# Kernel optimization log

Hardware: AMD Instinct MI355X
Metric: run time of the kernel (lower is better)

Reference implementation:

```python
import jax, jax.numpy as jnp
import numpy as np

# dims
B, T, C, D, H, NH, HD, INTER, L = 4, 1024, 256, 256, 512, 8, 64, 2048, 4
CF, CB, BASE = 0, 128, 10000.0  # context_forward, context_backward, rope theta


def _rope_tables():
    inv = 1.0 / (BASE ** (jnp.arange(0, HD, 2, dtype=jnp.float32) / HD))
    t = jnp.arange(T, dtype=jnp.float32)
    f = jnp.einsum('i,j->ij', t, inv)          # [T, HD/2]
    emb = jnp.concatenate([f, f], axis=-1)      # [T, HD]
    return jnp.cos(emb), jnp.sin(emb)


def _rotate_half(x):
    x1, x2 = jnp.split(x, 2, axis=-1)
    return jnp.concatenate([-x2, x1], axis=-1)


def _ln(x, g, b):
    m = x.mean(-1, keepdims=True)
    v = ((x - m) ** 2).mean(-1, keepdims=True)
    return (x - m) / jnp.sqrt(v + 1e-5) * g + b


def _band_mask():
    # create_context_mask(CF, CB, T): allow j in [i-CB, i+CF]
    i = jnp.arange(T)[:, None]
    j = jnp.arange(T)[None, :]
    return (j <= i + CF) & (j >= i - CB)  # [T, T] bool


def setup_inputs() -> dict:
    key = jax.random.key(0)
    ks = jax.random.split(key, 16)
    w = lambda k, shp: (0.02 * jax.random.normal(k, shp)).astype(jnp.float32)
    return {
        'spikes': jax.random.normal(ks[0], (B, T, C), dtype=jnp.float32),
        'spikes_mask': jnp.ones((B, T), dtype=jnp.int32),
        'spikes_timestamp': jnp.tile(jnp.arange(T, dtype=jnp.int32), (B, 1)),
        'embed_w': w(ks[1], (C, D)), 'embed_b': jnp.zeros((D,), jnp.float32),
        'proj_w': w(ks[2], (D, H)), 'proj_b': jnp.zeros((H,), jnp.float32),
        'ln1_g': jnp.ones((L, H), jnp.float32), 'ln1_b': jnp.zeros((L, H), jnp.float32),
        'Wq': w(ks[3], (L, H, H)), 'bq': jnp.zeros((L, H), jnp.float32),
        'Wk': w(ks[4], (L, H, H)), 'bk': jnp.zeros((L, H), jnp.float32),
        'Wv': w(ks[5], (L, H, H)), 'bv': jnp.zeros((L, H), jnp.float32),
        'Wo': w(ks[6], (L, H, H)), 'bo': jnp.zeros((L, H), jnp.float32),
        'ln2_g': jnp.ones((L, H), jnp.float32), 'ln2_b': jnp.zeros((L, H), jnp.float32),
        'up_w': w(ks[7], (L, H, INTER)), 'up_b': jnp.zeros((L, INTER), jnp.float32),
        'down_w': w(ks[8], (L, INTER, H)), 'down_b': jnp.zeros((L, H), jnp.float32),
    }


def reference(spikes, spikes_mask, spikes_timestamp, embed_w, embed_b, proj_w, proj_b,
              ln1_g, ln1_b, Wq, bq, Wk, bk, Wv, bv, Wo, bo, ln2_g, ln2_b,
              up_w, up_b, down_w, down_b):
    cos, sin = _rope_tables()
    mask = _band_mask()[None, None] & (spikes_mask[:, None, None, :] > 0)  # [B,1,T,T]
    cs = cos[spikes_timestamp][:, None]  # [B,1,T,HD]
    sn = sin[spikes_timestamp][:, None]
    neg = jnp.finfo(jnp.float32).min

    # NeuralEmbeddingLayer (no stack/pos/tokens): Linear -> gelu -> Linear
    x = jax.nn.gelu(spikes @ embed_w + embed_b, approximate=False) @ proj_w + proj_b

    for l in range(L):
        h = _ln(x, ln1_g[l], ln1_b[l])
        q = (h @ Wq[l] + bq[l]).reshape(B, T, NH, HD).transpose(0, 2, 1, 3)
        k = (h @ Wk[l] + bk[l]).reshape(B, T, NH, HD).transpose(0, 2, 1, 3)
        v = (h @ Wv[l] + bv[l]).reshape(B, T, NH, HD).transpose(0, 2, 1, 3)
        q = q * cs + _rotate_half(q) * sn
        k = k * cs + _rotate_half(k) * sn
        s = jnp.einsum('bhqd,bhkd->bhqk', q, k) / np.float32(np.sqrt(HD))
        s = jnp.where(mask, s, neg)
        p = jax.nn.softmax(s, axis=-1)
        o = jnp.einsum('bhqk,bhkd->bhqd', p, v).transpose(0, 2, 1, 3).reshape(B, T, H)
        x = x + o @ Wo[l] + bo[l]
        h = _ln(x, ln2_g[l], ln2_b[l])
        x = x + jax.nn.gelu(h @ up_w[l] + up_b[l], approximate=False) @ down_w[l] + down_b[l]
    return x
```

## Files before the change

### kernel.cpp

```cpp
#include <hip/hip_runtime.h>
#include <math.h>

#define B_ 4
#define T_ 1024
#define C_ 256
#define D_ 256
#define H_ 512
#define NH_ 8
#define HD_ 64
#define INTER_ 2048
#define L_ 4
#define CB_ 128

typedef short bf16x8 __attribute__((ext_vector_type(8)));
typedef float f32x4 __attribute__((ext_vector_type(4)));

__device__ __forceinline__ float gelu_exact(float x) {
    return 0.5f * x * (1.0f + erff(x * 0.70710678118654752f));
}

__device__ __forceinline__ unsigned short f2bf(float f) {
    unsigned u = __float_as_uint(f);
    u += 0x7fffu + ((u >> 16) & 1u);
    return (unsigned short)(u >> 16);
}
__device__ __forceinline__ float bf2f(unsigned short h) {
    return __uint_as_float((unsigned)h << 16);
}

__device__ __forceinline__ void xcd_swz(int& bx, int& by) {
    const int gx  = gridDim.x;
    const int nwg = gx * gridDim.y;
    int bid = blockIdx.y * gx + blockIdx.x;
    bid = (bid & 7) * (nwg >> 3) + (bid >> 3);
    bx = bid % gx;
    by = bid / gx;
}

template<int ACT, int RES, int OBF, int SPLIT>
__global__ __launch_bounds__(256) void mm64_k(
    const unsigned short* __restrict__ A, const unsigned short* __restrict__ BT,
    const float* __restrict__ b0, const float* __restrict__ b1,
    const float* __restrict__ b2,
    const float* res,
    void* o0, void* o1, void* o2,
    const int M, const int N, const int K)
{
    __shared__ unsigned short As[64 * 64];
    __shared__ unsigned short Bs[64 * 64];

    int bx, by; xcd_swz(bx, by);

    const int tid  = threadIdx.x;
    const int lane = tid & 63;
    const int w    = tid >> 6;
    const int m0   = by * 64;
    const int n0   = bx * 64;
    const int wm   = (w >> 1) * 32;
    const int wn   = (w & 1) * 32;
    const int l16  = lane & 15;
    const int g16  = lane >> 4;

    f32x4 acc[2][2] = {};

    const unsigned short* Abase = A  + (size_t)m0 * K;
    const unsigned short* Bbase = BT + (size_t)n0 * K;

    const int c0 = (w << 6) + lane;
    const int c1 = c0 + 256;
    const int r0c = c0 >> 3, g0c = c0 & 7, gk0 = g0c ^ (r0c & 7);
    const int r1c = c1 >> 3, g1c = c1 & 7, gk1 = g1c ^ (r1c & 7);

    for (int k0 = 0; k0 < K; k0 += 64) {
        __syncthreads();
        __builtin_amdgcn_global_load_lds(
            (const __attribute__((address_space(1))) unsigned*)(Abase + (size_t)r0c * K + k0 + gk0 * 8),
            (__attribute__((address_space(3))) unsigned*)(As + (size_t)(w << 6) * 8), 16, 0, 0);
        __builtin_amdgcn_global_load_lds(
            (const __attribute__((address_space(1))) unsigned*)(Abase + (size_t)r1c * K + k0 + gk1 * 8),
            (__attribute__((address_space(3))) unsigned*)(As + (size_t)(256 + (w << 6)) * 8), 16, 0, 0);
        __builtin_amdgcn_global_load_lds(
            (const __attribute__((address_space(1))) unsigned*)(Bbase + (size_t)r0c * K + k0 + gk0 * 8),
            (__attribute__((address_space(3))) unsigned*)(Bs + (size_t)(w << 6) * 8), 16, 0, 0);
        __builtin_amdgcn_global_load_lds(
            (const __attribute__((address_space(1))) unsigned*)(Bbase + (size_t)r1c * K + k0 + gk1 * 8),
            (__attribute__((address_space(3))) unsigned*)(Bs + (size_t)(256 + (w << 6)) * 8), 16, 0, 0);
        __syncthreads();

#pragma unroll
        for (int kk = 0; kk < 2; ++kk) {
            const int kf = kk * 4 + g16;
            const int sw = (kf ^ (l16 & 7)) * 8;
            bf16x8 a[2], b[2];
#pragma unroll
            for (int t = 0; t < 2; ++t)
                a[t] = *(const bf16x8*)&As[(wm + t * 16 + l16) * 64 + sw];
#pragma unroll
            for (int t = 0; t < 2; ++t)
                b[t] = *(const bf16x8*)&Bs[(wn + t * 16 + l16) * 64 + sw];
#pragma unroll
            for (int i = 0; i < 2; ++i)
#pragma unroll
                for (int j = 0; j < 2; ++j)
                    acc[i][j] = __builtin_amdgcn_mfma_f32_16x16x32_bf16(a[i], b[j], acc[i][j], 0, 0, 0);
        }
    }

    if (OBF || SPLIT) {
        __syncthreads();
        unsigned short* Eb = ((w < 2) ? As : Bs) + (w & 1) * 1024;
        const int row16 = lane >> 2;
        const int cg    = lane & 3;

        const int gnb   = n0 + wn;
        const int which = SPLIT ? (gnb >> 9) : 0;
        const int lnb   = SPLIT ? (gnb & 511) : gnb;
        const int ldo   = SPLIT ? 512 : N;
        unsigned short* oo = SPLIT
            ? ((which == 0) ? (unsigned short*)o0 : (which == 1) ? (unsigned short*)o1 : (unsigned short*)o2)
            : (unsigned short*)o0;
        const float* bb = SPLIT ? ((which == 0) ? b0 : (which == 1) ? b1 : b2) : b0;
        const float scale = (SPLIT && which == 0) ? 0.125f : 1.0f;

#pragma unroll
        for (int i = 0; i < 2; ++i) {
#pragma unroll
            for (int j = 0; j < 2; ++j) {
                const float bv = bb[lnb + j * 16 + l16];
#pragma unroll
                for (int r = 0; r < 4; ++r) {
                    float cv = acc[i][j][r] + bv;
                    if (ACT) cv = gelu_exact(cv);
                    if (SPLIT) cv *= scale;
                    Eb[(g16 * 4 + r) * 40 + j * 16 + l16] = f2bf(cv);
                }
            }
            const int grow0 = m0 + wm + i * 16 + row16;
#pragma unroll
            for (int s = 0; s < 2; ++s) {
                ushort4 t4 = *(const ushort4*)&Eb[row16 * 40 + s * 16 + cg * 4];
                *(ushort4*)&oo[(size_t)grow0 * ldo + lnb + s * 16 + cg * 4] = t4;
            }
        }
        return;
    }

#pragma unroll
    for (int i = 0; i < 2; ++i) {
        const int gmb = m0 + wm + i * 16 + g16 * 4;
#pragma unroll
        for (int j = 0; j < 2; ++j) {
            const int gn = n0 + wn + j * 16 + l16;
            const float bv = b0[gn];
#pragma unroll
            for (int r = 0; r < 4; ++r) {
                float cv = acc[i][j][r] + bv;
                if (ACT) cv = gelu_exact(cv);
                if (RES) cv += res[(size_t)(gmb + r) * 512 + gn];
                ((float*)o0)[(size_t)(gmb + r) * N + gn] = cv;
            }
        }
    }
}

template<int ACT, int RES, int OBF, int SPLIT>
__global__ __launch_bounds__(256) void mm128_k(
    const unsigned short* __restrict__ A, const unsigned short* __restrict__ BT,
    const float* __restrict__ b0, const float* __restrict__ b1,
    const float* __restrict__ b2,
    const float* res,
    void* o0, void* o1, void* o2,
    const int M, const int N, const int K)
{
    __shared__ unsigned short As[128 * 64];
    __shared__ unsigned short Bs[64 * 64];

    int bx, by; xcd_swz(bx, by);

    const int tid  = threadIdx.x;
    const int lane = tid & 63;
    const int w    = tid >> 6;
    const int m0   = by * 128;
    const int n0   = bx * 64;
    const int wm   = (w >> 1) * 64;
    const int wn   = (w & 1) * 32;
    const int l16  = lane & 15;
    const int g16  = lane >> 4;

    f32x4 acc[4][2] = {};

    const unsigned short* Abase = A  + (size_t)m0 * K;
    const unsigned short* Bbase = BT + (size_t)n0 * K;

    for (int k0 = 0; k0 < K; k0 += 64) {
        __syncthreads();
#pragma unroll
        for (int it = 0; it < 4; ++it) {
            const int c = it * 256 + tid;
            const int rc = c >> 3, gk = (c & 7) ^ (rc & 7);
            __builtin_amdgcn_global_load_lds(
                (const __attribute__((address_space(1))) unsigned*)(Abase + (size_t)rc * K + k0 + gk * 8),
                (__attribute__((address_space(3))) unsigned*)(As + (size_t)(it * 256 + (w << 6)) * 8), 16, 0, 0);
        }
#pragma unroll
        for (int it = 0; it < 2; ++it) {
            const int c = it * 256 + tid;
            const int rc = c >> 3, gk = (c & 7) ^ (rc & 7);
            __builtin_amdgcn_global_load_lds(
                (const __attribute__((address_space(1))) unsigned*)(Bbase + (size_t)rc * K + k0 + gk * 8),
                (__attribute__((address_space(3))) unsigned*)(Bs + (size_t)(it * 256 + (w << 6)) * 8), 16, 0, 0);
        }
        __syncthreads();

#pragma unroll
        for (int kk = 0; kk < 2; ++kk) {
            const int kf = kk * 4 + g16;
            const int sw = (kf ^ (l16 & 7)) * 8;
            bf16x8 a[4], b[2];
#pragma unroll
            for (int t = 0; t < 4; ++t)
                a[t] = *(const bf16x8*)&As[(wm + t * 16 + l16) * 64 + sw];
#pragma unroll
            for (int t = 0; t < 2; ++t)
                b[t] = *(const bf16x8*)&Bs[(wn + t * 16 + l16) * 64 + sw];
#pragma unroll
            for (int i = 0; i < 4; ++i)
#pragma unroll
                for (int j = 0; j < 2; ++j)
                    acc[i][j] = __builtin_amdgcn_mfma_f32_16x16x32_bf16(a[i], b[j], acc[i][j], 0, 0, 0);
        }
    }

    if (OBF || SPLIT) {
        __syncthreads();
        constexpr int EST = 40;
        unsigned short* Eb = As + w * (16 * EST);
        const int erow = lane >> 3;
        const int ecol = (lane & 7) * 4;

        const int gnb   = n0 + wn;
        const int which = SPLIT ? (gnb >> 9) : 0;
        const int lnb   = SPLIT ? (gnb & 511) : gnb;
        const int ldo   = SPLIT ? 512 : N;
        unsigned short* oo = SPLIT
            ? ((which == 0) ? (unsigned short*)o0 : (which == 1) ? (unsigned short*)o1 : (unsigned short*)o2)
            : (unsigned short*)o0;
        const float* bb = SPLIT ? ((which == 0) ? b0 : (which == 1) ? b1 : b2) : b0;
        const float scale = (SPLIT && which == 0) ? 0.125f : 1.0f;

#pragma unroll
        for (int i = 0; i < 4; ++i) {
#pragma unroll
            for (int j = 0; j < 2; ++j) {
                const float bv = bb[lnb + j * 16 + l16];
#pragma unroll
                for (int r = 0; r < 4; ++r) {
                    float cv = acc[i][j][r] + bv;
                    if (ACT) cv = gelu_exact(cv);
                    if (SPLIT) cv *= scale;
                    Eb[(g16 * 4 + r) * EST + j * 16 + l16] = f2bf(cv);
                }
            }
            const int grow0 = m0 + wm + i * 16;
#pragma unroll
            for (int s = 0; s < 2; ++s) {
                ushort4 t4 = *(const ushort4*)&Eb[(s * 8 + erow) * EST + ecol];
                *(ushort4*)&oo[(size_t)(grow0 + s * 8 + erow) * ldo + lnb + ecol] = t4;
            }
        }
        return;
    }

#pragma unroll
    for (int i = 0; i < 4; ++i) {
        const int gmb = m0 + wm + i * 16 + g16 * 4;
#pragma unroll
        for (int j = 0; j < 2; ++j) {
            const int gn = n0 + wn + j * 16 + l16;
            const float bv = b0[gn];
#pragma unroll
            for (int r = 0; r < 4; ++r) {
                float cv = acc[i][j][r] + bv;
                if (ACT) cv = gelu_exact(cv);
                if (RES) cv += res[(size_t)(gmb + r) * 512 + gn];
                ((float*)o0)[(size_t)(gmb + r) * N + gn] = cv;
            }
        }
    }
}

__global__ __launch_bounds__(256) void prep_k(
    const float* __restrict__ spikes,
    const float* __restrict__ embed_w, const float* __restrict__ proj_w,
    const float* __restrict__ Wq, const float* __restrict__ Wk,
    const float* __restrict__ Wv, const float* __restrict__ Wo,
    const float* __restrict__ up_w, const float* __restrict__ down_w,
    unsigned short* __restrict__ spbf,
    unsigned short* __restrict__ embT, unsigned short* __restrict__ projT,
    unsigned short* __restrict__ qkvT, unsigned short* __restrict__ woT,
    unsigned short* __restrict__ upT, unsigned short* __restrict__ downT)
{
    const int idx = blockIdx.x;
    const int tid = threadIdx.x;

    if (idx >= 3120) {
        const int base = (idx - 3120) * 4096 + tid * 16;
#pragma unroll
        for (int s = 0; s < 4; ++s) {
            float4 v = *(const float4*)&spikes[base + s * 4];
            ushort4 o = {f2bf(v.x), f2bf(v.y), f2bf(v.z), f2bf(v.w)};
            *(ushort4*)&spbf[base + s * 4] = o;
        }
        return;
    }

    const float* src; unsigned short* dst; int R, Cc, t;
    if (idx < 16)      { src = embed_w; dst = embT;  R = C_; Cc = D_; t = idx; }
    else if (idx < 48) { src = proj_w;  dst = projT; R = D_; Cc = H_; t = idx - 16; }
    else if (idx < 816) {
        const int j = idx - 48;
        const int wsel = j >> 8;
        const int l = (j & 255) >> 6;
        t = j & 63;
        src = ((wsel == 0) ? Wq : (wsel == 1) ? Wk : Wv) + (size_t)l * H_ * H_;
        dst = qkvT + (size_t)l * 3 * H_ * H_ + (size_t)wsel * H_ * H_;
        R = H_; Cc = H_;
    } else if (idx < 1072) {
        const int j = idx - 816; const int l = j >> 6; t = j & 63;
        src = Wo + (size_t)l * H_ * H_; dst = woT + (size_t)l * H_ * H_;
        R = H_; Cc = H_;
    } else if (idx < 2096) {
        const int j = idx - 1072; const int l = j >> 8; t = j & 255;
        src = up_w + (size_t)l * H_ * INTER_; dst = upT + (size_t)l * INTER_ * H_;
        R = H_; Cc = INTER_;
    } else {
        const int j = idx - 2096; const int l = j >> 8; t = j & 255;
        src = down_w + (size_t)l * INTER_ * H_; dst = downT + (size_t)l * H_ * INTER_;
        R = INTER_; Cc = H_;
    }
    const int ntx = Cc >> 6;
    const int c0 = (t % ntx) * 64, r0 = (t / ntx) * 64;

    __shared__ float tile[64][65];
    const int tr = tid >> 4, tc = (tid & 15) * 4;
#pragma unroll
    for (int i = 0; i < 4; ++i) {
        float4 v = *(const float4*)&src[(size_t)(r0 + tr + i * 16) * Cc + c0 + tc];
        tile[tr + i * 16][tc + 0] = v.x;
        tile[tr + i * 16][tc + 1] = v.y;
        tile[tr + i * 16][tc + 2] = v.z;
        tile[tr + i * 16][tc + 3] = v.w;
    }
    __syncthreads();
#pragma unroll
    for (int i = 0; i < 4; ++i) {
        const int n = tr + i * 16;
        ushort4 o;
        o.x = f2bf(tile[tc + 0][n]);
        o.y = f2bf(tile[tc + 1][n]);
        o.z = f2bf(tile[tc + 2][n]);
        o.w = f2bf(tile[tc + 3][n]);
        *(ushort4*)&dst[(size_t)(c0 + n) * R + r0 + tc] = o;
    }
}

__global__ __launch_bounds__(256) void ln_k(
    const float* __restrict__ x, const float* __restrict__ g,
    const float* __restrict__ b, unsigned short* __restrict__ out)
{
    const int row = blockIdx.x;
    const int tid = threadIdx.x;
    const float* xr = x + (size_t)row * H_;

    float v0 = xr[tid];
    float v1 = xr[tid + 256];

    float s = v0 + v1;
#pragma unroll
    for (int off = 32; off; off >>= 1) s += __shfl_xor(s, off);

    __shared__ float red[4];
    const int wave = tid >> 6;
    if ((tid & 63) == 0) red[wave] = s;
    __syncthreads();
    const float mean = (red[0] + red[1] + red[2] + red[3]) * (1.0f / (float)H_);

    const float d0 = v0 - mean, d1 = v1 - mean;
    float q = d0 * d0 + d1 * d1;
#pragma unroll
    for (int off = 32; off; off >>= 1) q += __shfl_xor(q, off);
    __syncthreads();
    if ((tid & 63) == 0) red[wave] = q;
    __syncthreads();
    const float var = (red[0] + red[1] + red[2] + red[3]) * (1.0f / (float)H_);
    const float rstd = rsqrtf(var + 1e-5f);

    out[(size_t)row * H_ + tid]       = f2bf(d0 * rstd * g[tid] + b[tid]);
    out[(size_t)row * H_ + tid + 256] = f2bf(d1 * rstd * g[tid + 256] + b[tid + 256]);
}

#define AWIN 192
#define AKS 72
#define AVS 200

__global__ __launch_bounds__(256) void attn_k(
    const unsigned short* __restrict__ q, const unsigned short* __restrict__ k,
    const unsigned short* __restrict__ v, const int* __restrict__ smask,
    const int* __restrict__ ts, unsigned short* __restrict__ o)
{
    __shared__ unsigned short Qs[64 * AKS];
    __shared__ unsigned short Ks[AWIN * AKS];
    __shared__ unsigned short Vt[64 * AVS];
    unsigned short* const Pb = Ks;

    const int blk = blockIdx.x;
    const int qt = blk & 15;
    const int h  = (blk >> 4) & 7;
    const int b  = blk >> 7;
    const int tid  = threadIdx.x;
    const int lane = tid & 63;
    const int w    = tid >> 6;
    const int l16  = lane & 15;
    const int g16  = lane >> 4;

    const int qlo = qt * 64;
    const int klo = (qlo >= CB_) ? (qlo - CB_) : 0;
    const int tb  = b * 1024;

    {
        const unsigned short* gq = q + ((size_t)(tb + qlo)) * 512 + h * 64;
        for (int c = tid; c < 64 * 8; c += 256) {
            const int row = c >> 3, c4 = (c & 7) * 4;
            ushort4 lo = *(const ushort4*)&gq[(size_t)row * 512 + c4];
            ushort4 hi = *(const ushort4*)&gq[(size_t)row * 512 + c4 + 32];
            const float tstamp = (float)ts[tb + qlo + row];
            ushort4 olo, ohi;
#pragma unroll
            for (int j2 = 0; j2 < 4; ++j2) {
                const float freq = __expf(-0.2878231366242558f * (float)(c4 + j2));
                const float ang = tstamp * freq;
                const float cc = __cosf(ang), ss = __sinf(ang);
                const float v1 = bf2f(((const unsigned short*)&lo)[j2]);
                const float v2 = bf2f(((const unsigned short*)&hi)[j2]);
                ((unsigned short*)&olo)[j2] = f2bf(v1 * cc - v2 * ss);
                ((unsigned short*)&ohi)[j2] = f2bf(v2 * cc + v1 * ss);
            }
            *(ushort4*)&Qs[row * AKS + c4]      = olo;
            *(ushort4*)&Qs[row * AKS + c4 + 32] = ohi;
        }
    }
    {
        const unsigned short* gk = k + ((size_t)(tb + klo)) * 512 + h * 64;
        for (int c = tid; c < AWIN * 8; c += 256) {
            const int row = c >> 3, c4 = (c & 7) * 4;
            ushort4 lo = *(const ushort4*)&gk[(size_t)row * 512 + c4];
            ushort4 hi = *(const ushort4*)&gk[(size_t)row * 512 + c4 + 32];
            const float tstamp = (float)ts[tb + klo + row];
            ushort4 olo, ohi;
#pragma unroll
            for (int j2 = 0; j2 < 4; ++j2) {
                const float freq = __expf(-0.2878231366242558f * (float)(c4 + j2));
                const float ang = tstamp * freq;
                const float cc = __cosf(ang), ss = __sinf(ang);
                const float v1 = bf2f(((const unsigned short*)&lo)[j2]);
                const float v2 = bf2f(((const unsigned short*)&hi)[j2]);
                ((unsigned short*)&olo)[j2] = f2bf(v1 * cc - v2 * ss);
                ((unsigned short*)&ohi)[j2] = f2bf(v2 * cc + v1 * ss);
            }
            *(ushort4*)&Ks[row * AKS + c4]      = olo;
            *(ushort4*)&Ks[row * AKS + c4 + 32] = ohi;
        }
    }
    {
        const unsigned short* gv = v + ((size_t)(tb + klo)) * 512 + h * 64;
        for (int c = tid; c < AWIN * 16; c += 256) {
            const int row = c >> 4, c4 = (c & 15) * 4;
            ushort4 vv = *(const ushort4*)&gv[(size_t)row * 512 + c4];
            Vt[(c4 + 0) * AVS + row] = vv.x;
            Vt[(c4 + 1) * AVS + row] = vv.y;
            Vt[(c4 + 2) * AVS + row] = vv.z;
            Vt[(c4 + 3) * AVS + row] = vv.w;
        }
    }
    __syncthreads();

    f32x4 accs[12];
    {
        const bf16x8 a0 = *(const bf16x8*)&Qs[(w * 16 + l16) * AKS + g16 * 8];
        const bf16x8 a1 = *(const bf16x8*)&Qs[(w * 16 + l16) * AKS + 32 + g16 * 8];
#pragma unroll
        for (int t = 0; t < 12; ++t) {
            const bf16x8 b0 = *(const bf16x8*)&Ks[(t * 16 + l16) * AKS + g16 * 8];
            const bf16x8 b1 = *(const bf16x8*)&Ks[(t * 16 + l16) * AKS + 32 + g16 * 8];
            f32x4 c = {};
            c = __builtin_amdgcn_mfma_f32_16x16x32_bf16(a0, b0, c, 0, 0, 0);
            c = __builtin_amdgcn_mfma_f32_16x16x32_bf16(a1, b1, c, 0, 0, 0);
            accs[t] = c;
        }
    }

    bool mk[12];
    int  jj[12];
#pragma unroll
    for (int t = 0; t < 12; ++t) {
        jj[t] = klo + t * 16 + l16;
        mk[t] = smask[tb + jj[t]] > 0;
    }

    float rs[4];
#pragma unroll
    for (int r = 0; r < 4; ++r) {
        const int i = qlo + 16 * w + g16 * 4 + r;
        float mx = -1e30f;
#pragma unroll
        for (int t = 0; t < 12; ++t) {
            const bool val = mk[t] && (jj[t] >= i - CB_) && (jj[t] <= i);
            mx = fmaxf(mx, val ? accs[t][r] : -1e30f);
        }
        mx = fmaxf(mx, __shfl_xor(mx, 1));
        mx = fmaxf(mx, __shfl_xor(mx, 2));
        mx = fmaxf(mx, __shfl_xor(mx, 4));
        mx = fmaxf(mx, __shfl_xor(mx, 8));
        float sum = 0.0f;
#pragma unroll
        for (int t = 0; t < 12; ++t) {
            const bool val = mk[t] && (jj[t] >= i - CB_) && (jj[t] <= i);
            const float p = val ? __expf(accs[t][r] - mx) : 0.0f;
            accs[t][r] = p;
            sum += p;
        }
        sum += __shfl_xor(sum, 1);
        sum += __shfl_xor(sum, 2);
        sum += __shfl_xor(sum, 4);
        sum += __shfl_xor(sum, 8);
        rs[r] = 1.0f / sum;
    }

    __syncthreads();

#pragma unroll
    for (int t = 0; t < 12; ++t)
#pragma unroll
        for (int r = 0; r < 4; ++r)
            Pb[(16 * w + g16 * 4 + r) * AVS + t * 16 + l16] = f2bf(accs[t][r]);

    f32x4 acco[4];
#pragma unroll
    for (int nt = 0; nt < 4; ++nt) {
        f32x4 c = {};
#pragma unroll
        for (int ks = 0; ks < 6; ++ks) {
            const bf16x8 a = *(const bf16x8*)&Pb[(16 * w + l16) * AVS + ks * 32 + g16 * 8];
            const bf16x8 bb = *(const bf16x8*)&Vt[(nt * 16 + l16) * AVS + ks * 32 + g16 * 8];
            c = __builtin_amdgcn_mfma_f32_16x16x32_bf16(a, bb, c, 0, 0, 0);
        }
        acco[nt] = c;
    }

    __syncthreads();
#pragma unroll
    for (int nt = 0; nt < 4; ++nt)
#pragma unroll
        for (int r = 0; r < 4; ++r)
            Pb[(16 * w + g16 * 4 + r) * AVS + nt * 16 + l16] = f2bf(acco[nt][r] * rs[r]);

    const int row16 = lane >> 2, cg = lane & 3;
    const int grow = tb + qlo + 16 * w + row16;
#pragma unroll
    for (int s = 0; s < 4; ++s) {
        ushort4 t4 = *(const ushort4*)&Pb[(16 * w + row16) * AVS + s * 16 + cg * 4];
        *(ushort4*)&o[(size_t)grow * 512 + h * 64 + s * 16 + cg * 4] = t4;
    }
}

extern "C" void kernel_launch(void* const* d_in, const int* in_sizes, int n_in,
                              void* d_out, int out_size, void* d_ws, size_t ws_size,
                              hipStream_t stream)
{
    const float* spikes  = (const float*)d_in[0];
    const int*   smask   = (const int*)d_in[1];
    const int*   ts      = (const int*)d_in[2];
    const float* embed_w = (const float*)d_in[3];
    const float* embed_b = (const float*)d_in[4];
    const float* proj_w  = (const float*)d_in[5];
    const float* proj_b  = (const float*)d_in[6];
    const float* ln1_g   = (const float*)d_in[7];
    const float* ln1_b   = (const float*)d_in[8];
    const float* Wq      = (const float*)d_in[9];
    const float* bq      = (const float*)d_in[10];
    const float* Wk      = (const float*)d_in[11];
    const float* bk      = (const float*)d_in[12];
    const float* Wv      = (const float*)d_in[13];
    const float* bv      = (const float*)d_in[14];
    const float* Wo      = (const float*)d_in[15];
    const float* bo      = (const float*)d_in[16];
    const float* ln2_g   = (const float*)d_in[17];
    const float* ln2_b   = (const float*)d_in[18];
    const float* up_w    = (const float*)d_in[19];
    const float* up_b    = (const float*)d_in[20];
    const float* down_w  = (const float*)d_in[21];
    const float* down_b  = (const float*)d_in[22];

    const int M = B_ * T_;

    char* p = (char*)d_ws;
    float* x = (float*)p;                       p += (size_t)M * H_ * 4;
    unsigned short* qb  = (unsigned short*)p;   p += (size_t)M * H_ * 2;
    unsigned short* kb  = (unsigned short*)p;   p += (size_t)M * H_ * 2;
    unsigned short* vb  = (unsigned short*)p;   p += (size_t)M * H_ * 2;
    unsigned short* hbf = (unsigned short*)p;   p += (size_t)M * H_ * 2;
    unsigned short* obf = (unsigned short*)p;   p += (size_t)M * H_ * 2;
    unsigned short* ibf = (unsigned short*)p;   p += (size_t)M * INTER_ * 2;
    unsigned short* tbf = (unsigned short*)p;   p += (size_t)M * D_ * 2;
    unsigned short* spbf  = (unsigned short*)p; p += (size_t)M * C_ * 2;
    unsigned short* embT  = (unsigned short*)p; p += (size_t)D_ * C_ * 2;
    unsigned short* projT = (unsigned short*)p; p += (size_t)H_ * D_ * 2;
    unsigned short* qkvT  = (unsigned short*)p; p += (size_t)L_ * 3 * H_ * H_ * 2;
    unsigned short* woT   = (unsigned short*)p; p += (size_t)L_ * H_ * H_ * 2;
    unsigned short* upT   = (unsigned short*)p; p += (size_t)L_ * INTER_ * H_ * 2;
    unsigned short* downT = (unsigned short*)p; p += (size_t)L_ * H_ * INTER_ * 2;

    prep_k<<<3376, 256, 0, stream>>>(
        spikes, embed_w, proj_w, Wq, Wk, Wv, Wo, up_w, down_w,
        spbf, embT, projT, qkvT, woT, upT, downT);

    mm64_k<1, 0, 1, 0><<<dim3(D_ / 64, M / 64), 256, 0, stream>>>(
        spbf, embT, embed_b, nullptr, nullptr, nullptr,
        tbf, nullptr, nullptr, M, D_, C_);
    mm64_k<0, 0, 0, 0><<<dim3(H_ / 64, M / 64), 256, 0, stream>>>(
        tbf, projT, proj_b, nullptr, nullptr, nullptr,
        x, nullptr, nullptr, M, H_, D_);

    for (int l = 0; l < L_; ++l) {
        const unsigned short* qkvT_l = qkvT + (size_t)l * 3 * H_ * H_;
        const unsigned short* woT_l  = woT  + (size_t)l * H_ * H_;
        const unsigned short* upT_l  = upT  + (size_t)l * INTER_ * H_;
        const unsigned short* dnT_l  = downT + (size_t)l * H_ * INTER_;

        ln_k<<<M, 256, 0, stream>>>(x, ln1_g + l * H_, ln1_b + l * H_, hbf);

        mm128_k<0, 0, 1, 1><<<dim3((3 * H_) / 64, M / 128), 256, 0, stream>>>(
            hbf, qkvT_l, bq + l * H_, bk + l * H_, bv + l * H_, nullptr,
            qb, kb, vb, M, 3 * H_, H_);

        attn_k<<<B_ * NH_ * (T_ / 64), 256, 0, stream>>>(qb, kb, vb, smask, ts, obf);

        mm64_k<0, 1, 0, 0><<<dim3(H_ / 64, M / 64), 256, 0, stream>>>(
            obf, woT_l, bo + l * H_, nullptr, nullptr, x,
            x, nullptr, nullptr, M, H_, H_);

        ln_k<<<M, 256, 0, stream>>>(x, ln2_g + l * H_, ln2_b + l * H_, hbf);

        mm128_k<1, 0, 1, 0><<<dim3(INTER_ / 64, M / 128), 256, 0, stream>>>(
            hbf, upT_l, up_b + l * INTER_, nullptr, nullptr, nullptr,
            ibf, nullptr, nullptr, M, INTER_, H_);

        float* dst = (l == L_ - 1) ? (float*)d_out : x;
        mm64_k<0, 1, 0, 0><<<dim3(H_ / 64, M / 64), 256, 0, stream>>>(
            ibf, dnT_l, down_b + l * H_, nullptr, nullptr, x,
            dst, nullptr, nullptr, M, H_, INTER_);
    }
}
```

Baseline: 516.1 us.

## Split-K down projection with atomic accumulation into a pre-initialized residual buffer

The down projection (K=2048) now runs with a 4-way split-K grid, and each slice atomically adds its partial tile into the output buffer. The second layernorm kernel pre-initializes that buffer with the residual plus down bias, and ping-pong residual buffers are introduced so the new output does not alias the input. The aim is to raise occupancy for a small-N, long-K GEMM that previously launched only 512 blocks. The attention kernel also gets an XCD-aware block remap. The cost is float atomics traffic and non-deterministic summation order.

```diff
diff --git a/kernel.cpp b/kernel.cpp
--- a/kernel.cpp
+++ b/kernel.cpp
@@ -28,16 +28,18 @@
     return __uint_as_float((unsigned)h << 16);
 }
 
-__device__ __forceinline__ void xcd_swz(int& bx, int& by) {
-    const int gx  = gridDim.x;
-    const int nwg = gx * gridDim.y;
-    int bid = blockIdx.y * gx + blockIdx.x;
+__device__ __forceinline__ void xcd_swz3(int& bx, int& by, int& bz) {
+    const int gx  = gridDim.x, gy = gridDim.y;
+    const int nwg = gx * gy * gridDim.z;
+    int bid = (blockIdx.z * gy + blockIdx.y) * gx + blockIdx.x;
     bid = (bid & 7) * (nwg >> 3) + (bid >> 3);
     bx = bid % gx;
-    by = bid / gx;
-}
-
-template<int ACT, int RES, int OBF, int SPLIT>
+    int r = bid / gx;
+    by = r % gy;
+    bz = r / gy;
+}
+
+template<int ACT, int RES, int OBF, int SPLIT, int ATOM>
 __global__ __launch_bounds__(256) void mm64_k(
     const unsigned short* __restrict__ A, const unsigned short* __restrict__ BT,
     const float* __restrict__ b0, const float* __restrict__ b1,
@@ -49,7 +51,7 @@
     __shared__ unsigned short As[64 * 64];
     __shared__ unsigned short Bs[64 * 64];
 
-    int bx, by; xcd_swz(bx, by);
+    int bx, by, bz; xcd_swz3(bx, by, bz);
 
     const int tid  = threadIdx.x;
     const int lane = tid & 63;
@@ -71,7 +73,11 @@
     const int r0c = c0 >> 3, g0c = c0 & 7, gk0 = g0c ^ (r0c & 7);
     const int r1c = c1 >> 3, g1c = c1 & 7, gk1 = g1c ^ (r1c & 7);
 
-    for (int k0 = 0; k0 < K; k0 += 64) {
+    const int Kslice = ATOM ? (K / (int)gridDim.z) : K;
+    const int kbeg   = ATOM ? bz * Kslice : 0;
+    const int kend   = kbeg + Kslice;
+
+    for (int k0 = kbeg; k0 < kend; k0 += 64) {
         __syncthreads();
         __builtin_amdgcn_global_load_lds(
             (const __attribute__((address_space(1))) unsigned*)(Abase + (size_t)r0c * K + k0 + gk0 * 8),
@@ -106,6 +112,22 @@
         }
     }
 
+    if (ATOM) {
+        float* out = (float*)o0;
+#pragma unroll
+        for (int i = 0; i < 2; ++i) {
+            const int gmb = m0 + wm + i * 16 + g16 * 4;
+#pragma unroll
+            for (int j = 0; j < 2; ++j) {
+                const int gn = n0 + wn + j * 16 + l16;
+#pragma unroll
+                for (int r = 0; r < 4; ++r)
+                    atomicAdd(&out[(size_t)(gmb + r) * N + gn], acc[i][j][r]);
+            }
+        }
+        return;
+    }
+
     if (OBF || SPLIT) {
         __syncthreads();
         unsigned short* Eb = ((w < 2) ? As : Bs) + (w & 1) * 1024;
@@ -175,7 +197,7 @@
     __shared__ unsigned short As[128 * 64];
     __shared__ unsigned short Bs[64 * 64];
 
-    int bx, by; xcd_swz(bx, by);
+    int bx, by, bz; xcd_swz3(bx, by, bz);
 
     const int tid  = threadIdx.x;
     const int lane = tid & 63;
@@ -364,9 +386,11 @@
     }
 }
 
+template<int INIT>
 __global__ __launch_bounds__(256) void ln_k(
     const float* __restrict__ x, const float* __restrict__ g,
-    const float* __restrict__ b, unsigned short* __restrict__ out)
+    const float* __restrict__ b, const float* __restrict__ db,
+    unsigned short* __restrict__ out, float* __restrict__ xb)
 {
     const int row = blockIdx.x;
     const int tid = threadIdx.x;
@@ -374,6 +398,11 @@
 
     float v0 = xr[tid];
     float v1 = xr[tid + 256];
+
+    if (INIT) {
+        xb[(size_t)row * H_ + tid]       = v0 + db[tid];
+        xb[(size_t)row * H_ + tid + 256] = v1 + db[tid + 256];
+    }
 
     float s = v0 + v1;
 #pragma unroll
@@ -413,7 +442,8 @@
     __shared__ unsigned short Vt[64 * AVS];
     unsigned short* const Pb = Ks;
 
-    const int blk = blockIdx.x;
+    int blk = blockIdx.x;
+    blk = (blk & 7) * ((int)gridDim.x >> 3) + (blk >> 3);
     const int qt = blk & 15;
     const int h  = (blk >> 4) & 7;
     const int b  = blk >> 7;
@@ -604,7 +634,8 @@
     const int M = B_ * T_;
 
     char* p = (char*)d_ws;
-    float* x = (float*)p;                       p += (size_t)M * H_ * 4;
+    float* x  = (float*)p;                      p += (size_t)M * H_ * 4;
+    float* x2 = (float*)p;                      p += (size_t)M * H_ * 4;
     unsigned short* qb  = (unsigned short*)p;   p += (size_t)M * H_ * 2;
     unsigned short* kb  = (unsigned short*)p;   p += (size_t)M * H_ * 2;
     unsigned short* vb  = (unsigned short*)p;   p += (size_t)M * H_ * 2;
@@ -624,12 +655,15 @@
         spikes, embed_w, proj_w, Wq, Wk, Wv, Wo, up_w, down_w,
         spbf, embT, projT, qkvT, woT, upT, downT);
 
-    mm64_k<1, 0, 1, 0><<<dim3(D_ / 64, M / 64), 256, 0, stream>>>(
+    mm64_k<1, 0, 1, 0, 0><<<dim3(D_ / 64, M / 64), 256, 0, stream>>>(
         spbf, embT, embed_b, nullptr, nullptr, nullptr,
         tbf, nullptr, nullptr, M, D_, C_);
-    mm64_k<0, 0, 0, 0><<<dim3(H_ / 64, M / 64), 256, 0, stream>>>(
+    mm64_k<0, 0, 0, 0, 0><<<dim3(H_ / 64, M / 64), 256, 0, stream>>>(
         tbf, projT, proj_b, nullptr, nullptr, nullptr,
         x, nullptr, nullptr, M, H_, D_);
+
+    float* cur = x;
+    float* alt = x2;
 
     for (int l = 0; l < L_; ++l) {
         const unsigned short* qkvT_l = qkvT + (size_t)l * 3 * H_ * H_;
@@ -637,7 +671,8 @@
         const unsigned short* upT_l  = upT  + (size_t)l * INTER_ * H_;
         const unsigned short* dnT_l  = downT + (size_t)l * H_ * INTER_;
 
-        ln_k<<<M, 256, 0, stream>>>(x, ln1_g + l * H_, ln1_b + l * H_, hbf);
+        ln_k<0><<<M, 256, 0, stream>>>(cur, ln1_g + l * H_, ln1_b + l * H_,
+                                       nullptr, hbf, nullptr);
 
         mm128_k<0, 0, 1, 1><<<dim3((3 * H_) / 64, M / 128), 256, 0, stream>>>(
             hbf, qkvT_l, bq + l * H_, bk + l * H_, bv + l * H_, nullptr,
@@ -645,19 +680,23 @@
 
         attn_k<<<B_ * NH_ * (T_ / 64), 256, 0, stream>>>(qb, kb, vb, smask, ts, obf);
 
-        mm64_k<0, 1, 0, 0><<<dim3(H_ / 64, M / 64), 256, 0, stream>>>(
-            obf, woT_l, bo + l * H_, nullptr, nullptr, x,
-            x, nullptr, nullptr, M, H_, H_);
-
-        ln_k<<<M, 256, 0, stream>>>(x, ln2_g + l * H_, ln2_b + l * H_, hbf);
+        mm64_k<0, 1, 0, 0, 0><<<dim3(H_ / 64, M / 64), 256, 0, stream>>>(
+            obf, woT_l, bo + l * H_, nullptr, nullptr, cur,
+            cur, nullptr, nullptr, M, H_, H_);
+
+        float* xd = (l == L_ - 1) ? (float*)d_out : alt;
+        ln_k<1><<<M, 256, 0, stream>>>(cur, ln2_g + l * H_, ln2_b + l * H_,
+                                       down_b + l * H_, hbf, xd);
 
         mm128_k<1, 0, 1, 0><<<dim3(INTER_ / 64, M / 128), 256, 0, stream>>>(
             hbf, upT_l, up_b + l * INTER_, nullptr, nullptr, nullptr,
             ibf, nullptr, nullptr, M, INTER_, H_);
 
-        float* dst = (l == L_ - 1) ? (float*)d_out : x;
-        mm64_k<0, 1, 0, 0><<<dim3(H_ / 64, M / 64), 256, 0, stream>>>(
-            ibf, dnT_l, down_b + l * H_, nullptr, nullptr, x,
-            dst, nullptr, nullptr, M, H_, INTER_);
-    }
-}
+        mm64_k<0, 0, 0, 0, 1><<<dim3(H_ / 64, M / 64, 4), 256, 0, stream>>>(
+            ibf, dnT_l, nullptr, nullptr, nullptr, nullptr,
+            xd, nullptr, nullptr, M, H_, INTER_);
+
+        alt = cur;
+        cur = xd;
+    }
+}
```

New measurement: 562.0 us. +8.9%, slower.

## Stage two K-slices per sync in GEMM; load rotated Q straight into registers

Applied to the files above, without the earlier changes.

The GEMM main loop now loads two 64-wide K slices into separate LDS buffers per iteration, which halves the number of barrier pairs per K and doubles LDS use per block. In attention, each lane reads its own Q fragment from global memory, applies RoPE in registers and feeds the MFMA directly, removing the Q shared-memory tile and its stores and reloads. This requires K to be a multiple of 128 and may lower occupancy because of the larger LDS footprint.

```diff
diff --git a/kernel.cpp b/kernel.cpp
--- a/kernel.cpp
+++ b/kernel.cpp
@@ -13,6 +13,7 @@
 #define CB_ 128
 
 typedef short bf16x8 __attribute__((ext_vector_type(8)));
+typedef unsigned short ush8 __attribute__((ext_vector_type(8)));
 typedef float f32x4 __attribute__((ext_vector_type(4)));
 
 __device__ __forceinline__ float gelu_exact(float x) {
@@ -46,8 +47,8 @@
     void* o0, void* o1, void* o2,
     const int M, const int N, const int K)
 {
-    __shared__ unsigned short As[64 * 64];
-    __shared__ unsigned short Bs[64 * 64];
+    __shared__ unsigned short As[2][64 * 64];
+    __shared__ unsigned short Bs[2][64 * 64];
 
     int bx, by; xcd_swz(bx, by);
 
@@ -68,47 +69,56 @@
 
     const int c0 = (w << 6) + lane;
     const int c1 = c0 + 256;
-    const int r0c = c0 >> 3, g0c = c0 & 7, gk0 = g0c ^ (r0c & 7);
-    const int r1c = c1 >> 3, g1c = c1 & 7, gk1 = g1c ^ (r1c & 7);
-
-    for (int k0 = 0; k0 < K; k0 += 64) {
+    const int r0c = c0 >> 3, gk0 = (c0 & 7) ^ (r0c & 7);
+    const int r1c = c1 >> 3, gk1 = (c1 & 7) ^ (r1c & 7);
+
+#define STAGE64(buf, kk0) do {                                                                        \
+    __builtin_amdgcn_global_load_lds(                                                                 \
+        (const __attribute__((address_space(1))) unsigned*)(Abase + (size_t)r0c * K + (kk0) + gk0 * 8), \
+        (__attribute__((address_space(3))) unsigned*)(As[buf] + (size_t)(w << 6) * 8), 16, 0, 0);     \
+    __builtin_amdgcn_global_load_lds(                                                                 \
+        (const __attribute__((address_space(1))) unsigned*)(Abase + (size_t)r1c * K + (kk0) + gk1 * 8), \
+        (__attribute__((address_space(3))) unsigned*)(As[buf] + (size_t)(256 + (w << 6)) * 8), 16, 0, 0); \
+    __builtin_amdgcn_global_load_lds(                                                                 \
+        (const __attribute__((address_space(1))) unsigned*)(Bbase + (size_t)r0c * K + (kk0) + gk0 * 8), \
+        (__attribute__((address_space(3))) unsigned*)(Bs[buf] + (size_t)(w << 6) * 8), 16, 0, 0);     \
+    __builtin_amdgcn_global_load_lds(                                                                 \
+        (const __attribute__((address_space(1))) unsigned*)(Bbase + (size_t)r1c * K + (kk0) + gk1 * 8), \
+        (__attribute__((address_space(3))) unsigned*)(Bs[buf] + (size_t)(256 + (w << 6)) * 8), 16, 0, 0); \
+} while (0)
+
+    for (int k0 = 0; k0 < K; k0 += 128) {
         __syncthreads();
-        __builtin_amdgcn_global_load_lds(
-            (const __attribute__((address_space(1))) unsigned*)(Abase + (size_t)r0c * K + k0 + gk0 * 8),
-            (__attribute__((address_space(3))) unsigned*)(As + (size_t)(w << 6) * 8), 16, 0, 0);
-        __builtin_amdgcn_global_load_lds(
-            (const __attribute__((address_space(1))) unsigned*)(Abase + (size_t)r1c * K + k0 + gk1 * 8),
-            (__attribute__((address_space(3))) unsigned*)(As + (size_t)(256 + (w << 6)) * 8), 16, 0, 0);
-        __builtin_amdgcn_global_load_lds(
-            (const __attribute__((address_space(1))) unsigned*)(Bbase + (size_t)r0c * K + k0 + gk0 * 8),
-            (__attribute__((address_space(3))) unsigned*)(Bs + (size_t)(w << 6) * 8), 16, 0, 0);
-        __builtin_amdgcn_global_load_lds(
-            (const __attribute__((address_space(1))) unsigned*)(Bbase + (size_t)r1c * K + k0 + gk1 * 8),
-            (__attribute__((address_space(3))) unsigned*)(Bs + (size_t)(256 + (w << 6)) * 8), 16, 0, 0);
+        STAGE64(0, k0);
+        STAGE64(1, k0 + 64);
         __syncthreads();
 
 #pragma unroll
-        for (int kk = 0; kk < 2; ++kk) {
-            const int kf = kk * 4 + g16;
-            const int sw = (kf ^ (l16 & 7)) * 8;
-            bf16x8 a[2], b[2];
-#pragma unroll
-            for (int t = 0; t < 2; ++t)
-                a[t] = *(const bf16x8*)&As[(wm + t * 16 + l16) * 64 + sw];
-#pragma unroll
-            for (int t = 0; t < 2; ++t)
-                b[t] = *(const bf16x8*)&Bs[(wn + t * 16 + l16) * 64 + sw];
-#pragma unroll
-            for (int i = 0; i < 2; ++i)
-#pragma unroll
-                for (int j = 0; j < 2; ++j)
-                    acc[i][j] = __builtin_amdgcn_mfma_f32_16x16x32_bf16(a[i], b[j], acc[i][j], 0, 0, 0);
-        }
-    }
+        for (int half = 0; half < 2; ++half) {
+#pragma unroll
+            for (int kk = 0; kk < 2; ++kk) {
+                const int kf = kk * 4 + g16;
+                const int sw = (kf ^ (l16 & 7)) * 8;
+                bf16x8 a[2], b[2];
+#pragma unroll
+                for (int t = 0; t < 2; ++t)
+                    a[t] = *(const bf16x8*)&As[half][(wm + t * 16 + l16) * 64 + sw];
+#pragma unroll
+                for (int t = 0; t < 2; ++t)
+                    b[t] = *(const bf16x8*)&Bs[half][(wn + t * 16 + l16) * 64 + sw];
+#pragma unroll
+                for (int i = 0; i < 2; ++i)
+#pragma unroll
+                    for (int j = 0; j < 2; ++j)
+                        acc[i][j] = __builtin_amdgcn_mfma_f32_16x16x32_bf16(a[i], b[j], acc[i][j], 0, 0, 0);
+            }
+        }
+    }
+#undef STAGE64
 
     if (OBF || SPLIT) {
         __syncthreads();
-        unsigned short* Eb = ((w < 2) ? As : Bs) + (w & 1) * 1024;
+        unsigned short* Eb = ((w < 2) ? As[0] : Bs[0]) + (w & 1) * 1024;
         const int row16 = lane >> 2;
         const int cg    = lane & 3;
 
@@ -408,7 +418,6 @@
     const unsigned short* __restrict__ v, const int* __restrict__ smask,
     const int* __restrict__ ts, unsigned short* __restrict__ o)
 {
-    __shared__ unsigned short Qs[64 * AKS];
     __shared__ unsigned short Ks[AWIN * AKS];
     __shared__ unsigned short Vt[64 * AVS];
     unsigned short* const Pb = Ks;
@@ -427,28 +436,26 @@
     const int klo = (qlo >= CB_) ? (qlo - CB_) : 0;
     const int tb  = b * 1024;
 
+    bf16x8 qa0, qa1;
     {
-        const unsigned short* gq = q + ((size_t)(tb + qlo)) * 512 + h * 64;
-        for (int c = tid; c < 64 * 8; c += 256) {
-            const int row = c >> 3, c4 = (c & 7) * 4;
-            ushort4 lo = *(const ushort4*)&gq[(size_t)row * 512 + c4];
-            ushort4 hi = *(const ushort4*)&gq[(size_t)row * 512 + c4 + 32];
-            const float tstamp = (float)ts[tb + qlo + row];
-            ushort4 olo, ohi;
-#pragma unroll
-            for (int j2 = 0; j2 < 4; ++j2) {
-                const float freq = __expf(-0.2878231366242558f * (float)(c4 + j2));
-                const float ang = tstamp * freq;
-                const float cc = __cosf(ang), ss = __sinf(ang);
-                const float v1 = bf2f(((const unsigned short*)&lo)[j2]);
-                const float v2 = bf2f(((const unsigned short*)&hi)[j2]);
-                ((unsigned short*)&olo)[j2] = f2bf(v1 * cc - v2 * ss);
-                ((unsigned short*)&ohi)[j2] = f2bf(v2 * cc + v1 * ss);
-            }
-            *(ushort4*)&Qs[row * AKS + c4]      = olo;
-            *(ushort4*)&Qs[row * AKS + c4 + 32] = ohi;
-        }
-    }
+        const int qrow = w * 16 + l16;
+        const unsigned short* gq = q + ((size_t)(tb + qlo + qrow)) * 512 + h * 64;
+        ush8 lo = *(const ush8*)&gq[g16 * 8];
+        ush8 hi = *(const ush8*)&gq[g16 * 8 + 32];
+        const float tstamp = (float)ts[tb + qlo + qrow];
+#pragma unroll
+        for (int j = 0; j < 8; ++j) {
+            const int d = g16 * 8 + j;
+            const float freq = __expf(-0.2878231366242558f * (float)d);
+            const float ang = tstamp * freq;
+            const float cc = __cosf(ang), ss = __sinf(ang);
+            const float v1 = bf2f(lo[j]);
+            const float v2 = bf2f(hi[j]);
+            ((unsigned short*)&qa0)[j] = f2bf(v1 * cc - v2 * ss);
+            ((unsigned short*)&qa1)[j] = f2bf(v2 * cc + v1 * ss);
+        }
+    }
+
     {
         const unsigned short* gk = k + ((size_t)(tb + klo)) * 512 + h * 64;
         for (int c = tid; c < AWIN * 8; c += 256) {
@@ -485,18 +492,14 @@
     __syncthreads();
 
     f32x4 accs[12];
-    {
-        const bf16x8 a0 = *(const bf16x8*)&Qs[(w * 16 + l16) * AKS + g16 * 8];
-        const bf16x8 a1 = *(const bf16x8*)&Qs[(w * 16 + l16) * AKS + 32 + g16 * 8];
-#pragma unroll
-        for (int t = 0; t < 12; ++t) {
-            const bf16x8 b0 = *(const bf16x8*)&Ks[(t * 16 + l16) * AKS + g16 * 8];
-            const bf16x8 b1 = *(const bf16x8*)&Ks[(t * 16 + l16) * AKS + 32 + g16 * 8];
-            f32x4 c = {};
-            c = __builtin_amdgcn_mfma_f32_16x16x32_bf16(a0, b0, c, 0, 0, 0);
-            c = __builtin_amdgcn_mfma_f32_16x16x32_bf16(a1, b1, c, 0, 0, 0);
-            accs[t] = c;
-        }
+#pragma unroll
+    for (int t = 0; t < 12; ++t) {
+        const bf16x8 b0 = *(const bf16x8*)&Ks[(t * 16 + l16) * AKS + g16 * 8];
+        const bf16x8 b1 = *(const bf16x8*)&Ks[(t * 16 + l16) * AKS + 32 + g16 * 8];
+        f32x4 c = {};
+        c = __builtin_amdgcn_mfma_f32_16x16x32_bf16(qa0, b0, c, 0, 0, 0);
+        c = __builtin_amdgcn_mfma_f32_16x16x32_bf16(qa1, b1, c, 0, 0, 0);
+        accs[t] = c;
     }
 
     bool mk[12];
```

Result: faster. 497.9 us (-3.5%).
